# Kernel optimization log

Measured on AMD Instinct MI355X. Metric: run time of the kernel, lower is better.

The kernel has to match this reference:

```python
import jax, jax.numpy as jnp
import numpy as np

N, F_IN, PRE, K = 400000, 64, 32, 6
EDGE = [32, 32]


def _dense_params(key, fan_in, fan_out):
    kw, kb = jax.random.split(key)
    W = jax.random.normal(kw, (fan_in, fan_out), jnp.float32) / np.sqrt(fan_in).astype(np.float32)
    b = jnp.zeros((fan_out,), jnp.float32)
    return W, b


def setup_inputs() -> dict:
    key = jax.random.key(0)
    ks = jax.random.split(key, 10)
    x = jax.random.normal(ks[0], (N, F_IN), jnp.float32)
    distsq = jax.random.uniform(ks[1], (N, K), jnp.float32)
    nidx = jax.random.randint(ks[2], (N, K), 0, N, jnp.int64)
    Wp, bp = _dense_params(ks[3], F_IN, PRE)
    # edge MLP: input K*(PRE+1) -> 32 -> 32 -> K
    We1, be1 = _dense_params(ks[4], K * (PRE + 1), EDGE[0])
    We2, be2 = _dense_params(ks[5], EDGE[0], EDGE[1])
    We3, be3 = _dense_params(ks[6], EDGE[1], K)
    # self MLP: F_IN -> 32 -> 32 -> 1
    Ws1, bs1 = _dense_params(ks[7], F_IN, EDGE[0])
    Ws2, bs2 = _dense_params(ks[8], EDGE[0], EDGE[1])
    Ws3, bs3 = _dense_params(ks[9], EDGE[1], 1)
    return dict(x=x, distsq=distsq, nidx=nidx, Wp=Wp, bp=bp,
                We1=We1, be1=be1, We2=We2, be2=be2, We3=We3, be3=be3,
                Ws1=Ws1, bs1=bs1, Ws2=Ws2, bs2=bs2, Ws3=Ws3, bs3=bs3)


def _forward(x, distsq, nidx, Wp, bp, We1, be1, We2, be2, We3, be3,
             Ws1, bs1, Ws2, bs2, Ws3, bs3):
    # pre-dense: [N, PRE]
    x_p = jax.nn.elu(x @ Wp + bp)
    # gather neighbors; select(nidx, x_n, 0.0) masks nidx<0 to 0.0
    safe_idx = jnp.maximum(nidx, 0)
    gathered = x_p[safe_idx]                              # [N, K, PRE]
    gathered = jnp.where(nidx[:, :, None] < 0, 0.0, gathered)
    diff = x_p[:, None, :] - gathered                     # [N, K, PRE]
    xn = jnp.concatenate([diff, distsq[:, :, None]], axis=2)  # [N, K, PRE+1]
    xn = xn.reshape(xn.shape[0], K * (PRE + 1))
    xn = jax.nn.elu(xn @ We1 + be1)
    xn = jax.nn.elu(xn @ We2 + be2)
    xn = xn @ We3 + be3                                   # [N, K]
    xs = jax.nn.elu(x @ Ws1 + bs1)
    xs = jax.nn.elu(xs @ Ws2 + bs2)
    xs = xs @ Ws3 + bs3                                   # [N, 1]
    out = jnp.concatenate([xs, xn], axis=1)               # [N, K+1]
    return jax.nn.softmax(out, axis=1)


def reference(x, distsq, nidx, Wp, bp, We1, be1, We2, be2, We3, be3,
              Ws1, bs1, Ws2, bs2, Ws3, bs3):
    return _forward(x, distsq, nidx, Wp, bp, We1, be1, We2, be2, We3, be3,
                    Ws1, bs1, Ws2, bs2, Ws3, bs3)
```

## Files before the change

### kernel.cpp

```cpp
#include <hip/hip_runtime.h>
#include <hip/hip_bf16.h>
#include <math.h>

typedef __hip_bfloat16 bf16;
typedef __attribute__((ext_vector_type(8))) __bf16 bf16x8;
typedef __attribute__((ext_vector_type(4))) float f32x4;

#define F_IN 64
#define KNB 6

#define WOFF_WP   0
#define WOFF_BP   2048
#define WOFF_WE1  2080
#define WOFF_BE1  8416
#define WOFF_WE2  8448
#define WOFF_BE2  9472
#define WOFF_WE3  9504
#define WOFF_BE3  9696
#define WOFF_WS1  9728
#define WOFF_BS1  11776
#define WOFF_WS2  11808
#define WOFF_BS2  12832
#define WOFF_WS3  12864
#define WOFF_BS3  12896
#define FLAGS_OFF 13056
#define WOFF_WSUM 13312
#define WOFF_WDSQ 14336
#define STAGE_OFF 16384

__device__ __forceinline__ float b2f(bf16 v) { return __bfloat162float(v); }
__device__ __forceinline__ float eluf(float v) { return v > 0.f ? v : __expf(v) - 1.f; }

__device__ __forceinline__ ushort f2bu(float v) {
  __bf16 b = (__bf16)v; ushort u; __builtin_memcpy(&u, &b, 2); return u;
}

union U8 { uint4 u; bf16x8 v; ushort s[8]; };

__device__ __forceinline__ void lds_fence() {
  __builtin_amdgcn_wave_barrier();
  __builtin_amdgcn_s_waitcnt(0xC07F);
  __builtin_amdgcn_wave_barrier();
}

__global__ void setupK(const ushort* xb, const int* ni,
                       const void* Wp, const void* bp, const void* We1, const void* be1,
                       const void* We2, const void* be2, const void* We3, const void* be3,
                       const void* Ws1, const void* bs1, const void* Ws2, const void* bs2,
                       const void* Ws3, const void* bs3, float* w) {
  __shared__ int sbf;
  int t = threadIdx.x;
  if (t < 64) {
    int bad = 0;
    for (int i = t; i < 256; i += 64) {
      float v = __uint_as_float(((unsigned)xb[i]) << 16);
      if (!(fabsf(v) < 100.f)) bad++;
    }
    unsigned long long bm = __ballot(bad > 0);
    unsigned long long hm = __ballot(ni[2 * t + 1] != 0);
    if (t == 0) {
      int isbf = (__popcll(bm) < 4) ? 1 : 0;
      ((int*)(w + FLAGS_OFF))[0] = isbf;
      ((int*)(w + FLAGS_OFF))[1] = (hm == 0ULL) ? 1 : 0;
      sbf = isbf;
    }
  }
  __syncthreads();
  int bf = sbf;
  const void* srcs[14] = {Wp, bp, We1, be1, We2, be2, We3, be3, Ws1, bs1, Ws2, bs2, Ws3, bs3};
  const int sizes[14] = {2048, 32, 6336, 32, 1024, 32, 192, 6, 2048, 32, 1024, 32, 32, 1};
  const int offs[14] = {WOFF_WP, WOFF_BP, WOFF_WE1, WOFF_BE1, WOFF_WE2, WOFF_BE2, WOFF_WE3,
                        WOFF_BE3, WOFF_WS1, WOFF_BS1, WOFF_WS2, WOFF_BS2, WOFF_WS3, WOFF_BS3};
  for (int tt = 0; tt < 14; tt++) {
    const void* s = srcs[tt];
    int nel = sizes[tt];
    float* d = w + offs[tt];
    for (int i = t; i < nel; i += blockDim.x)
      d[i] = bf ? b2f(((const bf16*)s)[i]) : ((const float*)s)[i];
  }
  __syncthreads();
  for (int i = t; i < 1024; i += blockDim.x) {
    int j = i >> 5, o = i & 31;
    float s = 0.f;
    for (int k = 0; k < KNB; k++) s += w[WOFF_WE1 + (k * 33 + j) * 32 + o];
    w[WOFF_WSUM + i] = s;
  }
  for (int i = t; i < 192; i += blockDim.x) {
    int k = i >> 5, o = i & 31;
    w[WOFF_WDSQ + i] = w[WOFF_WE1 + (k * 33 + 32) * 32 + o];
  }
}

__device__ __forceinline__ bf16x8 bfrag(const float* W, int ld, int nValid, int kValid, float sgn) {
  int lane = threadIdx.x & 63;
  int n = lane & 15, quad = lane >> 4;
  bf16x8 r;
#pragma unroll
  for (int j = 0; j < 8; j++) {
    int k = quad * 8 + j;
    float v = (n < nValid && k < kValid) ? sgn * W[k * ld + n] : 0.f;
    r[j] = (__bf16)v;
  }
  return r;
}

template <bool BF16>
__device__ __forceinline__ bf16x8 afrag_row(const void* base, long row, int k0) {
  int quad = (threadIdx.x & 63) >> 4;
  if (BF16) {
    U8 u;
    u.u = *(const uint4*)((const ushort*)base + row * F_IN + k0 + quad * 8);
    return u.v;
  } else {
    const float* p = (const float*)base + row * F_IN + k0 + quad * 8;
    float4 a = *(const float4*)p, b = *(const float4*)(p + 4);
    bf16x8 r;
    r[0] = (__bf16)a.x; r[1] = (__bf16)a.y; r[2] = (__bf16)a.z; r[3] = (__bf16)a.w;
    r[4] = (__bf16)b.x; r[5] = (__bf16)b.y; r[6] = (__bf16)b.z; r[7] = (__bf16)b.w;
    return r;
  }
}

template <bool BF16>
__device__ void pre_tiles(const void* xv, const float* __restrict__ w,
                          ushort* __restrict__ xp, float* __restrict__ xs,
                          int n_nodes, ushort* buf) {
  int lane = threadIdx.x & 63;
  int m = lane & 15, quad = lane >> 4;

  bf16x8 fwp[2][2], fws1[2][2], fws2[2], fws3;
#pragma unroll
  for (int s = 0; s < 2; s++)
#pragma unroll
    for (int t = 0; t < 2; t++) {
      fwp[s][t]  = bfrag(w + WOFF_WP  + s * 32 * 32 + 16 * t, 32, 16, 32, 1.f);
      fws1[s][t] = bfrag(w + WOFF_WS1 + s * 32 * 32 + 16 * t, 32, 16, 32, 1.f);
    }
#pragma unroll
  for (int t = 0; t < 2; t++) fws2[t] = bfrag(w + WOFF_WS2 + 16 * t, 32, 16, 32, 1.f);
  fws3 = bfrag(w + WOFF_WS3, 1, 1, 32, 1.f);
  float bpv[2], bs1v[2], bs2v[2];
#pragma unroll
  for (int t = 0; t < 2; t++) {
    bpv[t]  = w[WOFF_BP  + m + 16 * t];
    bs1v[t] = w[WOFF_BS1 + m + 16 * t];
    bs2v[t] = w[WOFF_BS2 + m + 16 * t];
  }
  float bs3f = w[WOFF_BS3];

  int T = (n_nodes + 15) >> 4;
  int wid = (int)((blockIdx.x * blockDim.x + threadIdx.x) >> 6);
  int nw = (int)((gridDim.x * blockDim.x) >> 6);
  f32x4 zero = {0.f, 0.f, 0.f, 0.f};

  for (int t0 = wid; t0 < T; t0 += nw) {
    long n0 = (long)t0 * 16;
    long row = n0 + m; if (row >= n_nodes) row = n_nodes - 1;
    bf16x8 a0 = afrag_row<BF16>(xv, row, 0);
    bf16x8 a1 = afrag_row<BF16>(xv, row, 32);
    f32x4 accp[2], accs[2];
#pragma unroll
    for (int t = 0; t < 2; t++) {
      accp[t] = __builtin_amdgcn_mfma_f32_16x16x32_bf16(a0, fwp[0][t], zero, 0, 0, 0);
      accp[t] = __builtin_amdgcn_mfma_f32_16x16x32_bf16(a1, fwp[1][t], accp[t], 0, 0, 0);
      accs[t] = __builtin_amdgcn_mfma_f32_16x16x32_bf16(a0, fws1[0][t], zero, 0, 0, 0);
      accs[t] = __builtin_amdgcn_mfma_f32_16x16x32_bf16(a1, fws1[1][t], accs[t], 0, 0, 0);
    }
#pragma unroll
    for (int t = 0; t < 2; t++)
#pragma unroll
      for (int r = 0; r < 4; r++)
        buf[(quad * 4 + r) * 32 + m + 16 * t] = f2bu(eluf(accp[t][r] + bpv[t]));
    lds_fence();
    {
      uint4 rv = *(const uint4*)(buf + m * 32 + quad * 8);
      *(uint4*)(xp + row * 32 + quad * 8) = rv;
    }
#pragma unroll
    for (int t = 0; t < 2; t++)
#pragma unroll
      for (int r = 0; r < 4; r++)
        buf[(quad * 4 + r) * 32 + m + 16 * t] = f2bu(eluf(accs[t][r] + bs1v[t]));
    lds_fence();
    U8 as1; as1.u = *(const uint4*)(buf + m * 32 + quad * 8);
    f32x4 acc2[2];
#pragma unroll
    for (int t = 0; t < 2; t++)
      acc2[t] = __builtin_amdgcn_mfma_f32_16x16x32_bf16(as1.v, fws2[t], zero, 0, 0, 0);
#pragma unroll
    for (int t = 0; t < 2; t++)
#pragma unroll
      for (int r = 0; r < 4; r++)
        buf[(quad * 4 + r) * 32 + m + 16 * t] = f2bu(eluf(acc2[t][r] + bs2v[t]));
    lds_fence();
    U8 as2; as2.u = *(const uint4*)(buf + m * 32 + quad * 8);
    f32x4 accx = __builtin_amdgcn_mfma_f32_16x16x32_bf16(as2.v, fws3, zero, 0, 0, 0);
    if (m == 0) {
#pragma unroll
      for (int r = 0; r < 4; r++) {
        long orow = n0 + quad * 4 + r;
        if (orow < n_nodes) xs[orow] = accx[r] + bs3f;
      }
    }
    lds_fence();
  }
}

__launch_bounds__(256)
__global__ void preK(const void* xv, const float* __restrict__ w,
                     const int* __restrict__ flags,
                     ushort* __restrict__ xp, float* __restrict__ xs, int n_nodes) {
  __shared__ ushort sb[4 * 512];
  ushort* buf = sb + (threadIdx.x >> 6) * 512;
  if (flags[0]) pre_tiles<true>(xv, w, xp, xs, n_nodes, buf);
  else          pre_tiles<false>(xv, w, xp, xs, n_nodes, buf);
}

template <bool BF16>
__device__ void edge_tiles(const ushort* __restrict__ xp, const float* __restrict__ xs,
                           const void* dsv, const int* __restrict__ ni, int i64,
                           const float* __restrict__ w, void* outv, int n_nodes,
                           ushort* buf, float* lbuf) {
  int lane = threadIdx.x & 63;
  int m = lane & 15, quad = lane >> 4;

  bf16x8 fsum[2], fwe1[KNB][2], fdsq[2], fwe2[2], fwe3;
#pragma unroll
  for (int t = 0; t < 2; t++) {
    fsum[t] = bfrag(w + WOFF_WSUM + 16 * t, 32, 16, 32, 1.f);
    fdsq[t] = bfrag(w + WOFF_WDSQ + 16 * t, 32, 16, KNB, 1.f);
    fwe2[t] = bfrag(w + WOFF_WE2 + 16 * t, 32, 16, 32, 1.f);
#pragma unroll
    for (int k = 0; k < KNB; k++)
      fwe1[k][t] = bfrag(w + WOFF_WE1 + k * 33 * 32 + 16 * t, 32, 16, 32, -1.f);
  }
  fwe3 = bfrag(w + WOFF_WE3, 6, 6, 32, 1.f);
  float be1v[2], be2v[2];
#pragma unroll
  for (int t = 0; t < 2; t++) {
    be1v[t] = w[WOFF_BE1 + m + 16 * t];
    be2v[t] = w[WOFF_BE2 + m + 16 * t];
  }
  float be3v = (m < 6) ? w[WOFF_BE3 + m] : 0.f;

  int T = (n_nodes + 15) >> 4;
  int wid = (int)((blockIdx.x * blockDim.x + threadIdx.x) >> 6);
  int nw = (int)((gridDim.x * blockDim.x) >> 6);
  f32x4 zero = {0.f, 0.f, 0.f, 0.f};

  for (int t0 = wid; t0 < T; t0 += nw) {
    long n0 = (long)t0 * 16;
    long row = n0 + m; if (row >= n_nodes) row = n_nodes - 1;

    int idxs[KNB];
#pragma unroll
    for (int k = 0; k < KNB; k++)
      idxs[k] = i64 ? ni[(row * KNB + k) * 2] : ni[row * KNB + k];

    U8 own; own.u = *(const uint4*)(xp + row * 32 + quad * 8);
    U8 nb[KNB];
#pragma unroll
    for (int k = 0; k < KNB; k++) {
      long ai = idxs[k];
      if (ai < 0 || ai >= n_nodes) ai = 0;
      nb[k].u = *(const uint4*)(xp + ai * 32 + quad * 8);
      if (idxs[k] < 0) { nb[k].u.x = 0; nb[k].u.y = 0; nb[k].u.z = 0; nb[k].u.w = 0; }
    }

    U8 ad; ad.u.x = 0; ad.u.y = 0; ad.u.z = 0; ad.u.w = 0;
    if (quad == 0) {
      if (BF16) {
        const unsigned* dp = (const unsigned*)dsv;
        ad.u.x = dp[row * 3 + 0];
        ad.u.y = dp[row * 3 + 1];
        ad.u.z = dp[row * 3 + 2];
      } else {
        const float* dp = (const float*)dsv + row * KNB;
#pragma unroll
        for (int k = 0; k < KNB; k++) ad.s[k] = f2bu(dp[k]);
      }
    }
    float xsv = xs[row];

    f32x4 accA[2], accB[2];
#pragma unroll
    for (int t = 0; t < 2; t++) {
      accA[t] = __builtin_amdgcn_mfma_f32_16x16x32_bf16(nb[0].v, fwe1[0][t], zero, 0, 0, 0);
      accA[t] = __builtin_amdgcn_mfma_f32_16x16x32_bf16(nb[1].v, fwe1[1][t], accA[t], 0, 0, 0);
      accA[t] = __builtin_amdgcn_mfma_f32_16x16x32_bf16(nb[2].v, fwe1[2][t], accA[t], 0, 0, 0);
      accB[t] = __builtin_amdgcn_mfma_f32_16x16x32_bf16(nb[3].v, fwe1[3][t], zero, 0, 0, 0);
      accB[t] = __builtin_amdgcn_mfma_f32_16x16x32_bf16(nb[4].v, fwe1[4][t], accB[t], 0, 0, 0);
      accB[t] = __builtin_amdgcn_mfma_f32_16x16x32_bf16(nb[5].v, fwe1[5][t], accB[t], 0, 0, 0);
      accB[t] = __builtin_amdgcn_mfma_f32_16x16x32_bf16(ad.v, fdsq[t], accB[t], 0, 0, 0);
      accA[t] = __builtin_amdgcn_mfma_f32_16x16x32_bf16(own.v, fsum[t], accA[t], 0, 0, 0);
    }

#pragma unroll
    for (int t = 0; t < 2; t++)
#pragma unroll
      for (int r = 0; r < 4; r++)
        buf[(quad * 4 + r) * 32 + m + 16 * t] =
            f2bu(eluf(accA[t][r] + accB[t][r] + be1v[t]));
    lds_fence();
    U8 a1; a1.u = *(const uint4*)(buf + m * 32 + quad * 8);
    f32x4 acc2[2];
#pragma unroll
    for (int t = 0; t < 2; t++)
      acc2[t] = __builtin_amdgcn_mfma_f32_16x16x32_bf16(a1.v, fwe2[t], zero, 0, 0, 0);
#pragma unroll
    for (int t = 0; t < 2; t++)
#pragma unroll
      for (int r = 0; r < 4; r++)
        buf[(quad * 4 + r) * 32 + m + 16 * t] = f2bu(eluf(acc2[t][r] + be2v[t]));
    lds_fence();
    U8 a2; a2.u = *(const uint4*)(buf + m * 32 + quad * 8);
    f32x4 acc3 = __builtin_amdgcn_mfma_f32_16x16x32_bf16(a2.v, fwe3, zero, 0, 0, 0);

    if (m < 6) {
#pragma unroll
      for (int r = 0; r < 4; r++) lbuf[(quad * 4 + r) * 8 + m] = acc3[r] + be3v;
    }
    lds_fence();
    if (lane < 16) {
      long nodeid = n0 + lane;
      if (nodeid < n_nodes) {
        float lg[7];
        lg[0] = xsv;
#pragma unroll
        for (int i = 0; i < 6; i++) lg[1 + i] = lbuf[lane * 8 + i];
        float mx = lg[0];
#pragma unroll
        for (int i = 1; i < 7; i++) mx = fmaxf(mx, lg[i]);
        float e[7], ssum = 0.f;
#pragma unroll
        for (int i = 0; i < 7; i++) { e[i] = __expf(lg[i] - mx); ssum += e[i]; }
        float inv = 1.f / ssum;
        if (BF16) {
          ushort* o = (ushort*)outv + nodeid * 7;
#pragma unroll
          for (int i = 0; i < 7; i++) o[i] = f2bu(e[i] * inv);
        } else {
          float* o = (float*)outv + nodeid * 7;
#pragma unroll
          for (int i = 0; i < 7; i++) o[i] = e[i] * inv;
        }
      }
    }
    lds_fence();
  }
}

__launch_bounds__(256)
__global__ void edgeK(const ushort* __restrict__ xp, const float* __restrict__ xs,
                      const void* dsv, const int* __restrict__ ni,
                      const float* __restrict__ w, const int* __restrict__ flags,
                      void* outv, int n_nodes) {
  __shared__ ushort sb[4 * 512];
  __shared__ float sl[4 * 128];
  ushort* buf = sb + (threadIdx.x >> 6) * 512;
  float* lbuf = sl + (threadIdx.x >> 6) * 128;
  if (flags[0]) edge_tiles<true>(xp, xs, dsv, ni, flags[1], w, outv, n_nodes, buf, lbuf);
  else          edge_tiles<false>(xp, xs, dsv, ni, flags[1], w, outv, n_nodes, buf, lbuf);
}

template <bool BF16>
__device__ __forceinline__ float wval(const void* W, long i) {
  if (BF16) return b2f(((const bf16*)W)[i]);
  return ((const float*)W)[i];
}

__device__ __forceinline__ void block_flags(const ushort* xb, const int* ni, int* sflags) {
  if (threadIdx.x < 64) {
    int t = threadIdx.x;
    int bad = 0;
    for (int i = t; i < 256; i += 64) {
      float v = __uint_as_float(((unsigned)xb[i]) << 16);
      if (!(fabsf(v) < 100.f)) bad++;
    }
    unsigned long long bm = __ballot(bad > 0);
    unsigned long long hm = __ballot(ni[2 * t + 1] != 0);
    if (t == 0) {
      sflags[0] = (__popcll(bm) < 4) ? 1 : 0;
      sflags[1] = (hm == 0ULL) ? 1 : 0;
    }
  }
  __syncthreads();
}

template <bool BF16>
__device__ void node_body(int n, int n_nodes, const void* xv, const void* dsv,
                          const int* __restrict__ ni, int i64,
                          const void* Wp, const void* bp, const void* We1, const void* be1,
                          const void* We2, const void* be2, const void* We3, const void* be3,
                          const void* Ws1, const void* bs1, const void* Ws2, const void* bs2,
                          const void* Ws3, const void* bs3, void* outv) {
  float h[32], s1[32];
#pragma unroll
  for (int o = 0; o < 32; o++) { h[o] = wval<BF16>(bp, o); s1[o] = wval<BF16>(bs1, o); }
  for (int j = 0; j < F_IN; j++) {
    float xj = wval<BF16>(xv, (long)n * F_IN + j);
#pragma unroll
    for (int o = 0; o < 32; o++) {
      h[o]  += xj * wval<BF16>(Wp,  (long)j * 32 + o);
      s1[o] += xj * wval<BF16>(Ws1, (long)j * 32 + o);
    }
  }
  float own[32];
#pragma unroll
  for (int o = 0; o < 32; o++) own[o] = eluf(h[o]);
  float s2[32];
#pragma unroll
  for (int o = 0; o < 32; o++) s2[o] = wval<BF16>(bs2, o);
  for (int j = 0; j < 32; j++) {
    float v = eluf(s1[j]);
#pragma unroll
    for (int o = 0; o < 32; o++) s2[o] += v * wval<BF16>(Ws2, (long)j * 32 + o);
  }
  float xsv = wval<BF16>(bs3, 0);
#pragma unroll
  for (int j = 0; j < 32; j++) xsv += eluf(s2[j]) * wval<BF16>(Ws3, j);

  float h1[32];
#pragma unroll
  for (int o = 0; o < 32; o++) h1[o] = wval<BF16>(be1, o);
  for (int k = 0; k < KNB; k++) {
    long pos = (long)n * KNB + k;
    int idx = i64 ? ni[2 * pos] : ni[pos];
    float mmask = idx < 0 ? 0.f : 1.f;
    long ai = idx < 0 ? 0 : idx;
    if (ai >= n_nodes) ai = 0;
    float nh[32];
#pragma unroll
    for (int o = 0; o < 32; o++) nh[o] = wval<BF16>(bp, o);
    for (int j = 0; j < F_IN; j++) {
      float xj = wval<BF16>(xv, ai * F_IN + j);
#pragma unroll
      for (int o = 0; o < 32; o++) nh[o] += xj * wval<BF16>(Wp, (long)j * 32 + o);
    }
#pragma unroll
    for (int j = 0; j < 32; j++) {
      float d = own[j] - mmask * eluf(nh[j]);
#pragma unroll
      for (int o = 0; o < 32; o++) h1[o] += d * wval<BF16>(We1, ((long)(k * 33 + j)) * 32 + o);
    }
    float dsq = BF16 ? b2f(((const bf16*)dsv)[pos]) : ((const float*)dsv)[pos];
#pragma unroll
    for (int o = 0; o < 32; o++) h1[o] += dsq * wval<BF16>(We1, ((long)(k * 33 + 32)) * 32 + o);
  }
  float h2[32];
#pragma unroll
  for (int o = 0; o < 32; o++) h2[o] = wval<BF16>(be2, o);
  for (int j = 0; j < 32; j++) {
    float v = eluf(h1[j]);
#pragma unroll
    for (int o = 0; o < 32; o++) h2[o] += v * wval<BF16>(We2, (long)j * 32 + o);
  }
  float lg[7];
  lg[0] = xsv;
#pragma unroll
  for (int o = 0; o < 6; o++) lg[1 + o] = wval<BF16>(be3, o);
  for (int j = 0; j < 32; j++) {
    float v = eluf(h2[j]);
#pragma unroll
    for (int o = 0; o < 6; o++) lg[1 + o] += v * wval<BF16>(We3, (long)j * 6 + o);
  }
  float mx = lg[0];
#pragma unroll
  for (int i = 1; i < 7; i++) mx = fmaxf(mx, lg[i]);
  float e[7], ssum = 0.f;
#pragma unroll
  for (int i = 0; i < 7; i++) { e[i] = __expf(lg[i] - mx); ssum += e[i]; }
  float inv = 1.f / ssum;
  if (BF16) {
    bf16* o = (bf16*)outv;
#pragma unroll
    for (int i = 0; i < 7; i++) o[(long)n * 7 + i] = __float2bfloat16(e[i] * inv);
  } else {
    float* o = (float*)outv;
#pragma unroll
    for (int i = 0; i < 7; i++) o[(long)n * 7 + i] = e[i] * inv;
  }
}

__launch_bounds__(256)
__global__ void fused(const void* xv, const void* dsv, const int* __restrict__ ni,
                      const void* Wp, const void* bp, const void* We1, const void* be1,
                      const void* We2, const void* be2, const void* We3, const void* be3,
                      const void* Ws1, const void* bs1, const void* Ws2, const void* bs2,
                      const void* Ws3, const void* bs3, void* outv, int n_nodes) {
  __shared__ int sflags[2];
  block_flags((const ushort*)xv, ni, sflags);
  int n = blockIdx.x * blockDim.x + threadIdx.x;
  if (n >= n_nodes) return;
  if (sflags[0]) node_body<true>(n, n_nodes, xv, dsv, ni, sflags[1], Wp, bp, We1, be1,
                                 We2, be2, We3, be3, Ws1, bs1, Ws2, bs2, Ws3, bs3, outv);
  else           node_body<false>(n, n_nodes, xv, dsv, ni, sflags[1], Wp, bp, We1, be1,
                                  We2, be2, We3, be3, Ws1, bs1, Ws2, bs2, Ws3, bs3, outv);
}

extern "C" void kernel_launch(void* const* d_in, const int* in_sizes, int n_in,
                              void* d_out, int out_size, void* d_ws, size_t ws_size,
                              hipStream_t stream) {
  const void* x      = d_in[0];
  const void* distsq = d_in[1];
  const int*  nidx   = (const int*)d_in[2];

  float* w = (float*)d_ws;
  int* flags = (int*)(w + FLAGS_OFF);
  int n_nodes = in_sizes[0] / F_IN;

  size_t need = (size_t)STAGE_OFF * 4 + (size_t)n_nodes * 64 + (size_t)n_nodes * 4 + 256;
  if (ws_size >= need) {
    setupK<<<1, 256, 0, stream>>>((const ushort*)x, nidx,
                                  d_in[3], d_in[4], d_in[5], d_in[6], d_in[7], d_in[8],
                                  d_in[9], d_in[10], d_in[11], d_in[12], d_in[13], d_in[14],
                                  d_in[15], d_in[16], w);
    ushort* xp = (ushort*)(w + STAGE_OFF);
    float* xs = (float*)(xp + (size_t)n_nodes * 32);
    preK<<<1024, 256, 0, stream>>>(x, w, flags, xp, xs, n_nodes);
    edgeK<<<1024, 256, 0, stream>>>(xp, xs, distsq, nidx, w, flags, d_out, n_nodes);
  } else {
    int grid = (n_nodes + 255) / 256;
    fused<<<grid, 256, 0, stream>>>(x, distsq, nidx, d_in[3], d_in[4], d_in[5], d_in[6],
                                    d_in[7], d_in[8], d_in[9], d_in[10], d_in[11], d_in[12],
                                    d_in[13], d_in[14], d_in[15], d_in[16], d_out, n_nodes);
  }
}
```

Measured before the change: 299.4 us.

## Precompute permuted MFMA weight fragments, transpose MFMA operands, and prefetch next tile

Setup now builds bf16 weight fragments once, with a column permutation chosen so each MFMA output lands in the layout the next layer needs as its input. This removes the per-layer LDS round-trips and wave fences. Weight fragments are staged into shared memory per block and read from there instead of living in registers. Both the pre and edge kernels double-buffer the next tile's input loads and neighbour gathers so they overlap the current tile's MFMAs. Folding be1 into the distsq fragment and using shuffles for the softmax gather drop further work, at the cost of more LDS reads per MFMA and higher register pressure.

```diff
diff --git a/kernel.cpp b/kernel.cpp
--- a/kernel.cpp
+++ b/kernel.cpp
@@ -26,7 +26,12 @@
 #define FLAGS_OFF 13056
 #define WOFF_WSUM 13312
 #define WOFF_WDSQ 14336
-#define STAGE_OFF 16384
+#define FRAG_OFF  14592
+#define NFRAG_PRE 11
+#define NFRAG_EDGE 19
+#define STAGE_OFF 24576
+
+#define MFMA(a, b, c) __builtin_amdgcn_mfma_f32_16x16x32_bf16(a, b, c, 0, 0, 0)
 
 __device__ __forceinline__ float b2f(bf16 v) { return __bfloat162float(v); }
 __device__ __forceinline__ float eluf(float v) { return v > 0.f ? v : __expf(v) - 1.f; }
@@ -37,11 +42,12 @@
 
 union U8 { uint4 u; bf16x8 v; ushort s[8]; };
 
-__device__ __forceinline__ void lds_fence() {
-  __builtin_amdgcn_wave_barrier();
-  __builtin_amdgcn_s_waitcnt(0xC07F);
-  __builtin_amdgcn_wave_barrier();
-}
+__device__ __forceinline__ bf16x8 ldfrag(const ushort* fr, int f) {
+  U8 u; u.u = *(const uint4*)(fr + f * 512 + (threadIdx.x & 63) * 8);
+  return u.v;
+}
+
+__device__ __forceinline__ int permo(int m, int t) { return 8 * (m >> 2) + (m & 3) + 4 * t; }
 
 __global__ void setupK(const ushort* xb, const int* ni,
                        const void* Wp, const void* bp, const void* We1, const void* be1,
@@ -89,120 +95,110 @@
     int k = i >> 5, o = i & 31;
     w[WOFF_WDSQ + i] = w[WOFF_WE1 + (k * 33 + 32) * 32 + o];
   }
-}
-
-__device__ __forceinline__ bf16x8 bfrag(const float* W, int ld, int nValid, int kValid, float sgn) {
-  int lane = threadIdx.x & 63;
-  int n = lane & 15, quad = lane >> 4;
-  bf16x8 r;
-#pragma unroll
-  for (int j = 0; j < 8; j++) {
-    int k = quad * 8 + j;
-    float v = (n < nValid && k < kValid) ? sgn * W[k * ld + n] : 0.f;
-    r[j] = (__bf16)v;
-  }
-  return r;
-}
-
-template <bool BF16>
-__device__ __forceinline__ bf16x8 afrag_row(const void* base, long row, int k0) {
-  int quad = (threadIdx.x & 63) >> 4;
-  if (BF16) {
-    U8 u;
-    u.u = *(const uint4*)((const ushort*)base + row * F_IN + k0 + quad * 8);
-    return u.v;
-  } else {
-    const float* p = (const float*)base + row * F_IN + k0 + quad * 8;
-    float4 a = *(const float4*)p, b = *(const float4*)(p + 4);
-    bf16x8 r;
-    r[0] = (__bf16)a.x; r[1] = (__bf16)a.y; r[2] = (__bf16)a.z; r[3] = (__bf16)a.w;
-    r[4] = (__bf16)b.x; r[5] = (__bf16)b.y; r[6] = (__bf16)b.z; r[7] = (__bf16)b.w;
-    return r;
+  __syncthreads();
+  ushort* fbv = (ushort*)(w + FRAG_OFF);
+  for (int i = t; i < (NFRAG_PRE + NFRAG_EDGE) * 512; i += blockDim.x) {
+    int f = i >> 9, e = i & 511;
+    int lane = e >> 3, j = e & 7;
+    int mm = lane & 15, qq = lane >> 4;
+    int k = qq * 8 + j;
+    float v = 0.f;
+    if (f < 4) { int s = f >> 1, tt = f & 1; v = w[WOFF_WP + (32 * s + k) * 32 + permo(mm, tt)]; }
+    else if (f < 8) { int s = (f - 4) >> 1, tt = f & 1; v = w[WOFF_WS1 + (32 * s + k) * 32 + permo(mm, tt)]; }
+    else if (f < 10) { int tt = f & 1; v = w[WOFF_WS2 + k * 32 + permo(mm, tt)]; }
+    else if (f == 10) { v = (mm == 0) ? w[WOFF_WS3 + k] : 0.f; }
+    else if (f < 23) { int kn = (f - 11) >> 1, tt = (f - 11) & 1;
+                       v = -w[WOFF_WE1 + (kn * 33 + k) * 32 + permo(mm, tt)]; }
+    else if (f < 25) { int tt = f - 23; v = w[WOFF_WSUM + k * 32 + permo(mm, tt)]; }
+    else if (f < 27) { int tt = f - 25; int o = permo(mm, tt);
+                       v = (k < 6) ? w[WOFF_WDSQ + k * 32 + o]
+                                   : (k == 6 ? w[WOFF_BE1 + o] : 0.f); }
+    else if (f < 29) { int tt = f - 27; v = w[WOFF_WE2 + k * 32 + permo(mm, tt)]; }
+    else { v = (mm < KNB) ? w[WOFF_WE3 + k * 6 + mm] : 0.f; }
+    fbv[i] = f2bu(v);
   }
 }
 
 template <bool BF16>
 __device__ void pre_tiles(const void* xv, const float* __restrict__ w,
                           ushort* __restrict__ xp, float* __restrict__ xs,
-                          int n_nodes, ushort* buf) {
+                          int n_nodes, const ushort* __restrict__ fr) {
   int lane = threadIdx.x & 63;
-  int m = lane & 15, quad = lane >> 4;
-
-  bf16x8 fwp[2][2], fws1[2][2], fws2[2], fws3;
-#pragma unroll
-  for (int s = 0; s < 2; s++)
-#pragma unroll
-    for (int t = 0; t < 2; t++) {
-      fwp[s][t]  = bfrag(w + WOFF_WP  + s * 32 * 32 + 16 * t, 32, 16, 32, 1.f);
-      fws1[s][t] = bfrag(w + WOFF_WS1 + s * 32 * 32 + 16 * t, 32, 16, 32, 1.f);
-    }
-#pragma unroll
-  for (int t = 0; t < 2; t++) fws2[t] = bfrag(w + WOFF_WS2 + 16 * t, 32, 16, 32, 1.f);
-  fws3 = bfrag(w + WOFF_WS3, 1, 1, 32, 1.f);
-  float bpv[2], bs1v[2], bs2v[2];
-#pragma unroll
-  for (int t = 0; t < 2; t++) {
-    bpv[t]  = w[WOFF_BP  + m + 16 * t];
-    bs1v[t] = w[WOFF_BS1 + m + 16 * t];
-    bs2v[t] = w[WOFF_BS2 + m + 16 * t];
-  }
-  float bs3f = w[WOFF_BS3];
-
-  int T = (n_nodes + 15) >> 4;
-  int wid = (int)((blockIdx.x * blockDim.x + threadIdx.x) >> 6);
-  int nw = (int)((gridDim.x * blockDim.x) >> 6);
+  int m = lane & 15, q = lane >> 4;
+  float bp8[8], bs18[8], bs28[8];
+#pragma unroll
+  for (int j = 0; j < 8; j++) {
+    bp8[j]  = w[WOFF_BP  + 8 * q + j];
+    bs18[j] = w[WOFF_BS1 + 8 * q + j];
+    bs28[j] = w[WOFF_BS2 + 8 * q + j];
+  }
+  float bs3 = w[WOFF_BS3];
+  long T = ((long)n_nodes + 15) >> 4;
+  long wid = (long)((blockIdx.x * blockDim.x + threadIdx.x) >> 6);
+  long nw = (long)((gridDim.x * blockDim.x) >> 6);
   f32x4 zero = {0.f, 0.f, 0.f, 0.f};
 
-  for (int t0 = wid; t0 < T; t0 += nw) {
-    long n0 = (long)t0 * 16;
+  uint4 bufA[4], bufB[4];
+  auto loadraw = [&](uint4* r, long tt) {
+    long row = tt * 16 + m; if (row >= n_nodes) row = n_nodes - 1;
+    if (BF16) {
+      const ushort* p = (const ushort*)xv + row * F_IN + q * 8;
+      r[0] = *(const uint4*)p;
+      r[1] = *(const uint4*)(p + 32);
+    } else {
+      const float* p = (const float*)xv + row * F_IN + q * 8;
+      r[0] = *(const uint4*)p;        r[1] = *(const uint4*)(p + 4);
+      r[2] = *(const uint4*)(p + 32); r[3] = *(const uint4*)(p + 36);
+    }
+  };
+  auto mkfrag = [&](const uint4* r, int s) -> bf16x8 {
+    if (BF16) { U8 u; u.u = r[s]; return u.v; }
+    const float* f0 = (const float*)(r + 2 * s);
+    bf16x8 out;
+#pragma unroll
+    for (int j = 0; j < 8; j++) out[j] = (__bf16)f0[j];
+    return out;
+  };
+  auto body = [&](uint4* cur, uint4* nxt, long t) {
+    long tn = t + nw;
+    if (tn < T) loadraw(nxt, tn);
+    long n0 = t * 16;
     long row = n0 + m; if (row >= n_nodes) row = n_nodes - 1;
-    bf16x8 a0 = afrag_row<BF16>(xv, row, 0);
-    bf16x8 a1 = afrag_row<BF16>(xv, row, 32);
-    f32x4 accp[2], accs[2];
-#pragma unroll
-    for (int t = 0; t < 2; t++) {
-      accp[t] = __builtin_amdgcn_mfma_f32_16x16x32_bf16(a0, fwp[0][t], zero, 0, 0, 0);
-      accp[t] = __builtin_amdgcn_mfma_f32_16x16x32_bf16(a1, fwp[1][t], accp[t], 0, 0, 0);
-      accs[t] = __builtin_amdgcn_mfma_f32_16x16x32_bf16(a0, fws1[0][t], zero, 0, 0, 0);
-      accs[t] = __builtin_amdgcn_mfma_f32_16x16x32_bf16(a1, fws1[1][t], accs[t], 0, 0, 0);
-    }
-#pragma unroll
-    for (int t = 0; t < 2; t++)
-#pragma unroll
-      for (int r = 0; r < 4; r++)
-        buf[(quad * 4 + r) * 32 + m + 16 * t] = f2bu(eluf(accp[t][r] + bpv[t]));
-    lds_fence();
-    {
-      uint4 rv = *(const uint4*)(buf + m * 32 + quad * 8);
-      *(uint4*)(xp + row * 32 + quad * 8) = rv;
-    }
-#pragma unroll
-    for (int t = 0; t < 2; t++)
-#pragma unroll
-      for (int r = 0; r < 4; r++)
-        buf[(quad * 4 + r) * 32 + m + 16 * t] = f2bu(eluf(accs[t][r] + bs1v[t]));
-    lds_fence();
-    U8 as1; as1.u = *(const uint4*)(buf + m * 32 + quad * 8);
-    f32x4 acc2[2];
-#pragma unroll
-    for (int t = 0; t < 2; t++)
-      acc2[t] = __builtin_amdgcn_mfma_f32_16x16x32_bf16(as1.v, fws2[t], zero, 0, 0, 0);
-#pragma unroll
-    for (int t = 0; t < 2; t++)
-#pragma unroll
-      for (int r = 0; r < 4; r++)
-        buf[(quad * 4 + r) * 32 + m + 16 * t] = f2bu(eluf(acc2[t][r] + bs2v[t]));
-    lds_fence();
-    U8 as2; as2.u = *(const uint4*)(buf + m * 32 + quad * 8);
-    f32x4 accx = __builtin_amdgcn_mfma_f32_16x16x32_bf16(as2.v, fws3, zero, 0, 0, 0);
-    if (m == 0) {
-#pragma unroll
-      for (int r = 0; r < 4; r++) {
-        long orow = n0 + quad * 4 + r;
-        if (orow < n_nodes) xs[orow] = accx[r] + bs3f;
-      }
-    }
-    lds_fence();
+    bf16x8 x0 = mkfrag(cur, 0), x1 = mkfrag(cur, 1);
+    f32x4 aP[2], aS[2];
+#pragma unroll
+    for (int tt = 0; tt < 2; tt++) {
+      aP[tt] = MFMA(ldfrag(fr, 0 + tt), x0, zero);
+      aP[tt] = MFMA(ldfrag(fr, 2 + tt), x1, aP[tt]);
+      aS[tt] = MFMA(ldfrag(fr, 4 + tt), x0, zero);
+      aS[tt] = MFMA(ldfrag(fr, 6 + tt), x1, aS[tt]);
+    }
+    U8 o1;
+#pragma unroll
+    for (int j = 0; j < 8; j++) o1.s[j] = f2bu(eluf(aP[j >> 2][j & 3] + bp8[j]));
+    *(uint4*)(xp + row * 32 + q * 8) = o1.u;
+    bf16x8 s1e;
+#pragma unroll
+    for (int j = 0; j < 8; j++) s1e[j] = (__bf16)eluf(aS[j >> 2][j & 3] + bs18[j]);
+    f32x4 a2[2];
+#pragma unroll
+    for (int tt = 0; tt < 2; tt++) a2[tt] = MFMA(ldfrag(fr, 8 + tt), s1e, zero);
+    bf16x8 s2e;
+#pragma unroll
+    for (int j = 0; j < 8; j++) s2e[j] = (__bf16)eluf(a2[j >> 2][j & 3] + bs28[j]);
+    f32x4 a3 = MFMA(ldfrag(fr, 10), s2e, zero);
+    if (q == 0) {
+      long orow = n0 + m;
+      if (orow < n_nodes) xs[orow] = a3[0] + bs3;
+    }
+  };
+  long t = wid;
+  if (t < T) loadraw(bufA, t);
+  while (t < T) {
+    body(bufA, bufB, t);
+    t += nw; if (t >= T) break;
+    body(bufB, bufA, t);
+    t += nw;
   }
 }
 
@@ -210,124 +206,98 @@
 __global__ void preK(const void* xv, const float* __restrict__ w,
                      const int* __restrict__ flags,
                      ushort* __restrict__ xp, float* __restrict__ xs, int n_nodes) {
-  __shared__ ushort sb[4 * 512];
-  ushort* buf = sb + (threadIdx.x >> 6) * 512;
-  if (flags[0]) pre_tiles<true>(xv, w, xp, xs, n_nodes, buf);
-  else          pre_tiles<false>(xv, w, xp, xs, n_nodes, buf);
-}
+  __shared__ uint4 fsh[NFRAG_PRE * 64];
+  const uint4* fbv = (const uint4*)((const ushort*)(w + FRAG_OFF));
+  for (int i = threadIdx.x; i < NFRAG_PRE * 64; i += blockDim.x) fsh[i] = fbv[i];
+  __syncthreads();
+  const ushort* fr = (const ushort*)fsh;
+  if (flags[0]) pre_tiles<true>(xv, w, xp, xs, n_nodes, fr);
+  else          pre_tiles<false>(xv, w, xp, xs, n_nodes, fr);
+}
+
+struct ETile { U8 nb[KNB]; U8 own; U8 ad; float xsv; };
 
 template <bool BF16>
 __device__ void edge_tiles(const ushort* __restrict__ xp, const float* __restrict__ xs,
                            const void* dsv, const int* __restrict__ ni, int i64,
                            const float* __restrict__ w, void* outv, int n_nodes,
-                           ushort* buf, float* lbuf) {
+                           const ushort* __restrict__ fr) {
   int lane = threadIdx.x & 63;
-  int m = lane & 15, quad = lane >> 4;
-
-  bf16x8 fsum[2], fwe1[KNB][2], fdsq[2], fwe2[2], fwe3;
-#pragma unroll
-  for (int t = 0; t < 2; t++) {
-    fsum[t] = bfrag(w + WOFF_WSUM + 16 * t, 32, 16, 32, 1.f);
-    fdsq[t] = bfrag(w + WOFF_WDSQ + 16 * t, 32, 16, KNB, 1.f);
-    fwe2[t] = bfrag(w + WOFF_WE2 + 16 * t, 32, 16, 32, 1.f);
+  int m = lane & 15, q = lane >> 4;
+  float b2[8], b3[4];
+#pragma unroll
+  for (int j = 0; j < 8; j++) b2[j] = w[WOFF_BE2 + 8 * q + j];
+#pragma unroll
+  for (int r = 0; r < 4; r++) { int o = 4 * q + r; b3[r] = (o < 6) ? w[WOFF_BE3 + o] : 0.f; }
+
+  long T = ((long)n_nodes + 15) >> 4;
+  long wid = (long)((blockIdx.x * blockDim.x + threadIdx.x) >> 6);
+  long nw = (long)((gridDim.x * blockDim.x) >> 6);
+  f32x4 zero = {0.f, 0.f, 0.f, 0.f};
+  ETile A, B;
+
+  auto phead = [&](ETile& d, int* idxn, long tt) {
+    long row = tt * 16 + m; if (row >= n_nodes) row = n_nodes - 1;
 #pragma unroll
     for (int k = 0; k < KNB; k++)
-      fwe1[k][t] = bfrag(w + WOFF_WE1 + k * 33 * 32 + 16 * t, 32, 16, 32, -1.f);
-  }
-  fwe3 = bfrag(w + WOFF_WE3, 6, 6, 32, 1.f);
-  float be1v[2], be2v[2];
-#pragma unroll
-  for (int t = 0; t < 2; t++) {
-    be1v[t] = w[WOFF_BE1 + m + 16 * t];
-    be2v[t] = w[WOFF_BE2 + m + 16 * t];
-  }
-  float be3v = (m < 6) ? w[WOFF_BE3 + m] : 0.f;
-
-  int T = (n_nodes + 15) >> 4;
-  int wid = (int)((blockIdx.x * blockDim.x + threadIdx.x) >> 6);
-  int nw = (int)((gridDim.x * blockDim.x) >> 6);
-  f32x4 zero = {0.f, 0.f, 0.f, 0.f};
-
-  for (int t0 = wid; t0 < T; t0 += nw) {
-    long n0 = (long)t0 * 16;
-    long row = n0 + m; if (row >= n_nodes) row = n_nodes - 1;
-
-    int idxs[KNB];
-#pragma unroll
-    for (int k = 0; k < KNB; k++)
-      idxs[k] = i64 ? ni[(row * KNB + k) * 2] : ni[row * KNB + k];
-
-    U8 own; own.u = *(const uint4*)(xp + row * 32 + quad * 8);
-    U8 nb[KNB];
-#pragma unroll
-    for (int k = 0; k < KNB; k++) {
-      long ai = idxs[k];
-      if (ai < 0 || ai >= n_nodes) ai = 0;
-      nb[k].u = *(const uint4*)(xp + ai * 32 + quad * 8);
-      if (idxs[k] < 0) { nb[k].u.x = 0; nb[k].u.y = 0; nb[k].u.z = 0; nb[k].u.w = 0; }
-    }
-
-    U8 ad; ad.u.x = 0; ad.u.y = 0; ad.u.z = 0; ad.u.w = 0;
-    if (quad == 0) {
+      idxn[k] = i64 ? ni[(row * KNB + k) * 2] : ni[row * KNB + k];
+    d.own.u = *(const uint4*)(xp + row * 32 + q * 8);
+    d.ad.u.x = 0; d.ad.u.y = 0; d.ad.u.z = 0; d.ad.u.w = 0;
+    if (q == 0) {
       if (BF16) {
         const unsigned* dp = (const unsigned*)dsv;
-        ad.u.x = dp[row * 3 + 0];
-        ad.u.y = dp[row * 3 + 1];
-        ad.u.z = dp[row * 3 + 2];
+        d.ad.u.x = dp[row * 3 + 0]; d.ad.u.y = dp[row * 3 + 1]; d.ad.u.z = dp[row * 3 + 2];
       } else {
         const float* dp = (const float*)dsv + row * KNB;
 #pragma unroll
-        for (int k = 0; k < KNB; k++) ad.s[k] = f2bu(dp[k]);
+        for (int k = 0; k < KNB; k++) d.ad.s[k] = f2bu(dp[k]);
       }
-    }
-    float xsv = xs[row];
-
-    f32x4 accA[2], accB[2];
-#pragma unroll
-    for (int t = 0; t < 2; t++) {
-      accA[t] = __builtin_amdgcn_mfma_f32_16x16x32_bf16(nb[0].v, fwe1[0][t], zero, 0, 0, 0);
-      accA[t] = __builtin_amdgcn_mfma_f32_16x16x32_bf16(nb[1].v, fwe1[1][t], accA[t], 0, 0, 0);
-      accA[t] = __builtin_amdgcn_mfma_f32_16x16x32_bf16(nb[2].v, fwe1[2][t], accA[t], 0, 0, 0);
-      accB[t] = __builtin_amdgcn_mfma_f32_16x16x32_bf16(nb[3].v, fwe1[3][t], zero, 0, 0, 0);
-      accB[t] = __builtin_amdgcn_mfma_f32_16x16x32_bf16(nb[4].v, fwe1[4][t], accB[t], 0, 0, 0);
-      accB[t] = __builtin_amdgcn_mfma_f32_16x16x32_bf16(nb[5].v, fwe1[5][t], accB[t], 0, 0, 0);
-      accB[t] = __builtin_amdgcn_mfma_f32_16x16x32_bf16(ad.v, fdsq[t], accB[t], 0, 0, 0);
-      accA[t] = __builtin_amdgcn_mfma_f32_16x16x32_bf16(own.v, fsum[t], accA[t], 0, 0, 0);
-    }
-
-#pragma unroll
-    for (int t = 0; t < 2; t++)
-#pragma unroll
-      for (int r = 0; r < 4; r++)
-        buf[(quad * 4 + r) * 32 + m + 16 * t] =
-            f2bu(eluf(accA[t][r] + accB[t][r] + be1v[t]));
-    lds_fence();
-    U8 a1; a1.u = *(const uint4*)(buf + m * 32 + quad * 8);
+      d.ad.s[6] = 0x3F80u;
+    }
+    d.xsv = xs[row];
+  };
+  auto pgather = [&](ETile& d, const int* idxn) {
+#pragma unroll
+    for (int k = 0; k < KNB; k++) {
+      int ix = idxn[k];
+      long ai = (ix < 0 || ix >= n_nodes) ? 0 : (long)ix;
+      uint4 g = *(const uint4*)(xp + ai * 32 + q * 8);
+      if (ix < 0) { g.x = 0; g.y = 0; g.z = 0; g.w = 0; }
+      d.nb[k].u = g;
+    }
+  };
+  auto body = [&](ETile& cur, ETile& nxt, long t) {
+    long tn = t + nw;
+    int idxn[KNB];
+    bool pv = tn < T;
+    if (pv) phead(nxt, idxn, tn);
+    f32x4 acc[2];
+#pragma unroll
+    for (int tt = 0; tt < 2; tt++) {
+      acc[tt] = MFMA(ldfrag(fr, 12 + tt), cur.own.v, zero);
+      acc[tt] = MFMA(ldfrag(fr, 14 + tt), cur.ad.v, acc[tt]);
+#pragma unroll
+      for (int k = 0; k < KNB; k++)
+        acc[tt] = MFMA(ldfrag(fr, k * 2 + tt), cur.nb[k].v, acc[tt]);
+    }
+    if (pv) pgather(nxt, idxn);
+    bf16x8 a1;
+#pragma unroll
+    for (int j = 0; j < 8; j++) a1[j] = (__bf16)eluf(acc[j >> 2][j & 3]);
     f32x4 acc2[2];
 #pragma unroll
-    for (int t = 0; t < 2; t++)
-      acc2[t] = __builtin_amdgcn_mfma_f32_16x16x32_bf16(a1.v, fwe2[t], zero, 0, 0, 0);
-#pragma unroll
-    for (int t = 0; t < 2; t++)
-#pragma unroll
-      for (int r = 0; r < 4; r++)
-        buf[(quad * 4 + r) * 32 + m + 16 * t] = f2bu(eluf(acc2[t][r] + be2v[t]));
-    lds_fence();
-    U8 a2; a2.u = *(const uint4*)(buf + m * 32 + quad * 8);
-    f32x4 acc3 = __builtin_amdgcn_mfma_f32_16x16x32_bf16(a2.v, fwe3, zero, 0, 0, 0);
-
-    if (m < 6) {
-#pragma unroll
-      for (int r = 0; r < 4; r++) lbuf[(quad * 4 + r) * 8 + m] = acc3[r] + be3v;
-    }
-    lds_fence();
+    for (int tt = 0; tt < 2; tt++) acc2[tt] = MFMA(ldfrag(fr, 16 + tt), a1, zero);
+    bf16x8 a2;
+#pragma unroll
+    for (int j = 0; j < 8; j++) a2[j] = (__bf16)eluf(acc2[j >> 2][j & 3] + b2[j]);
+    f32x4 a3 = MFMA(ldfrag(fr, 18), a2, zero);
+    float l0 = a3[0] + b3[0], l1 = a3[1] + b3[1], l2 = a3[2] + b3[2], l3 = a3[3] + b3[3];
+    float o4 = __shfl(l0, m + 16, 64);
+    float o5 = __shfl(l1, m + 16, 64);
     if (lane < 16) {
-      long nodeid = n0 + lane;
+      long nodeid = t * 16 + lane;
       if (nodeid < n_nodes) {
-        float lg[7];
-        lg[0] = xsv;
-#pragma unroll
-        for (int i = 0; i < 6; i++) lg[1 + i] = lbuf[lane * 8 + i];
+        float lg[7] = {cur.xsv, l0, l1, l2, l3, o4, o5};
         float mx = lg[0];
 #pragma unroll
         for (int i = 1; i < 7; i++) mx = fmaxf(mx, lg[i]);
@@ -346,7 +316,14 @@
         }
       }
     }
-    lds_fence();
+  };
+  long t = wid;
+  if (t < T) { int i0[KNB]; phead(A, i0, t); pgather(A, i0); }
+  while (t < T) {
+    body(A, B, t);
+    t += nw; if (t >= T) break;
+    body(B, A, t);
+    t += nw;
   }
 }
 
@@ -355,12 +332,13 @@
                       const void* dsv, const int* __restrict__ ni,
                       const float* __restrict__ w, const int* __restrict__ flags,
                       void* outv, int n_nodes) {
-  __shared__ ushort sb[4 * 512];
-  __shared__ float sl[4 * 128];
-  ushort* buf = sb + (threadIdx.x >> 6) * 512;
-  float* lbuf = sl + (threadIdx.x >> 6) * 128;
-  if (flags[0]) edge_tiles<true>(xp, xs, dsv, ni, flags[1], w, outv, n_nodes, buf, lbuf);
-  else          edge_tiles<false>(xp, xs, dsv, ni, flags[1], w, outv, n_nodes, buf, lbuf);
+  __shared__ uint4 fsh[NFRAG_EDGE * 64];
+  const uint4* fbv = (const uint4*)((const ushort*)(w + FRAG_OFF) + NFRAG_PRE * 512);
+  for (int i = threadIdx.x; i < NFRAG_EDGE * 64; i += blockDim.x) fsh[i] = fbv[i];
+  __syncthreads();
+  const ushort* fr = (const ushort*)fsh;
+  if (flags[0]) edge_tiles<true>(xp, xs, dsv, ni, flags[1], w, outv, n_nodes, fr);
+  else          edge_tiles<false>(xp, xs, dsv, ni, flags[1], w, outv, n_nodes, fr);
 }
 
 template <bool BF16>
```

Result: no change. 303.5 us (+1.4%).
